# Kernel tuning notes

Hardware: AMD Instinct MI355X
Metric: run time of the kernel (lower is better)

## Reference

```python
import jax, jax.numpy as jnp
import numpy as np

NUM_INPUTS = 16
NUM_HIDDEN = 256
NUM_LAYERS = 4
B = 16384


def setup_inputs() -> dict:
    key = jax.random.key(0)
    ks = jax.random.split(key, 8)
    H, N, L = NUM_HIDDEN, NUM_INPUTS, NUM_LAYERS
    x0 = jax.random.normal(ks[0], (B, N), dtype=jnp.float32)
    # input layer: Linear(2 -> H)
    W_in = jax.random.normal(ks[1], (2, H), dtype=jnp.float32) * (1.0 / np.sqrt(2.0))
    b_in = jnp.zeros((H,), dtype=jnp.float32)
    # L-1 intermediate layers: Linear(2H -> H), stacked
    W_mid = jax.random.normal(ks[2], (L - 1, 2 * H, H), dtype=jnp.float32) * (1.0 / np.sqrt(2.0 * H))
    b_mid = jnp.zeros((L - 1, H), dtype=jnp.float32)
    # slater: Linear(H -> N) with xavier-normal weight, zero bias
    W_sl = jax.random.normal(ks[3], (H, N), dtype=jnp.float32) * np.sqrt(2.0 / (H + N))
    b_sl = jnp.zeros((N,), dtype=jnp.float32)
    width = jnp.full((1,), 0.1, dtype=jnp.float32)
    return {"x0": x0, "W_in": W_in, "b_in": b_in, "W_mid": W_mid,
            "b_mid": b_mid, "W_sl": W_sl, "b_sl": b_sl, "width": width}


def _forward(x0, W_in, b_in, W_mid, b_mid, W_sl, b_sl, width):
    N = x0.shape[1]
    # input equivariant layer: f = stack(h, mean(h)) -> [B, N, 2]
    g = jnp.broadcast_to(x0.mean(axis=1, keepdims=True), x0.shape)
    f = jnp.stack((x0, g), axis=2)                       # [B, N, 2]
    h = jnp.tanh(jnp.einsum('bnf,fh->bnh', f, W_in) + b_in)  # [B, N, H]
    # intermediate equivariant layers with residual
    for i in range(W_mid.shape[0]):
        gm = jnp.broadcast_to(h.mean(axis=1, keepdims=True), h.shape)
        fm = jnp.concatenate((h, gm), axis=2)            # [B, N, 2H]
        h = jnp.tanh(jnp.einsum('bnf,fh->bnh', fm, W_mid[i]) + b_mid[i]) + h
    # slog slater determinant
    slater = jnp.einsum('bnh,hm->bnm', h, W_sl) + b_sl   # [B, N, N]
    sign, logabsdet = jnp.linalg.slogdet(slater)
    log_factorial = jnp.log(jnp.arange(1, N + 1, dtype=jnp.float32)).sum()
    log_bcs = -width[0] * jnp.sum(x0 ** 2, axis=1)       # [B]
    return sign, logabsdet - 0.5 * log_factorial + log_bcs


def reference(x0, W_in, b_in, W_mid, b_mid, W_sl, b_sl, width):
    return _forward(x0, W_in, b_in, W_mid, b_mid, W_sl, b_sl, width)
```

## Files before the change

### kernel.cpp

```cpp
#include <hip/hip_runtime.h>

#define BTOT 16384
#define NI   16
#define HD   256
#define BB   4
#define NMID 3
#define ASH  264
#define SLS  20
#define HALF_LOGFACT 15.3359295387f

typedef short  bf16x8 __attribute__((ext_vector_type(8)));
typedef float  f32x4  __attribute__((ext_vector_type(4)));

__device__ __forceinline__ unsigned short f2bf(float f) {
    unsigned u = __builtin_bit_cast(unsigned, f);
    u += 0x7FFFu + ((u >> 16) & 1u);
    return (unsigned short)(u >> 16);
}
__device__ __forceinline__ unsigned cvt_pk_bf16(float lo, float hi) {
    unsigned d;
    asm("v_cvt_pk_bf16_f32 %0, %1, %2" : "=v"(d) : "v"(lo), "v"(hi));
    return d;
}
__device__ __forceinline__ float bflo(unsigned u) { return __builtin_bit_cast(float, u << 16); }
__device__ __forceinline__ float bfhi(unsigned u) { return __builtin_bit_cast(float, u & 0xFFFF0000u); }
__device__ __forceinline__ float bcast(float x, int lane) {
    return __builtin_bit_cast(float,
        __builtin_amdgcn_readlane(__builtin_bit_cast(int, x), lane));
}
__device__ __forceinline__ float tanh5(float x) {
    float z = __builtin_amdgcn_exp2f(x * 2.885390081777927f);
    return __builtin_fmaf(-2.0f, __builtin_amdgcn_rcpf(1.0f + z), 1.0f);
}
#define LGKM_BAR() do { asm volatile("s_waitcnt lgkmcnt(0)" ::: "memory"); \
    __builtin_amdgcn_s_barrier(); __builtin_amdgcn_sched_barrier(0); } while (0)
#define LGKM_WAIT() do { asm volatile("s_waitcnt lgkmcnt(0)" ::: "memory"); \
    __builtin_amdgcn_sched_barrier(0); } while (0)

__global__ void prep_w(const float* __restrict__ Wmid, const float* __restrict__ Wsl,
                       unsigned short* __restrict__ wtc) {
    const int b = blockIdx.x;
    const int t = threadIdx.x;
    unsigned short* dst = wtc + (size_t)b * 8192;
    if (b < 48) {
        const int layer = b >> 4, ch = b & 15;
        const float* src = Wmid + (size_t)layer * (2 * HD * HD);
#pragma unroll 4
        for (int v = 0; v < 32; ++v) {
            int o = t * 32 + v;
            int kk = o & 7, j = (o >> 3) & 15, kg = o >> 7;
            dst[o] = f2bf(src[(8 * kg + kk) * HD + ch * 16 + j]);
        }
    } else {
#pragma unroll 4
        for (int v = 0; v < 32; ++v) {
            int o = t * 32 + v;
            int kk = o & 7, j = (o >> 3) & 15, kg = o >> 7;
            dst[o] = (kg < 32) ? f2bf(Wsl[(8 * kg + kk) * NI + j]) : (unsigned short)0;
        }
    }
}

struct __align__(16) SMem {
    union {
        unsigned short h[BB * NI * ASH];
        float slf[BB][NI * ASH / 2];
    } u;
    unsigned short stash[2 * NI * ASH];
    unsigned short gmgv[BB * HD];
};
static_assert(sizeof(SMem) == 52736, "R6-proven 3-blocks/CU size");

__global__ __launch_bounds__(256, 3)
void eqslater_mfma(const float* __restrict__ x0g,
                   const float* __restrict__ Win,
                   const float* __restrict__ bin,
                   const float* __restrict__ bmid,
                   const float* __restrict__ bsl,
                   const float* __restrict__ width,
                   const unsigned short* __restrict__ wtc,
                   float* __restrict__ out) {
    __shared__ SMem sm;
    const int tid = threadIdx.x;
    const int bbase = blockIdx.x * BB;
    const int w = tid >> 6;
    const int l = tid & 63;
    const int c = l & 15;
    const int g = l >> 4;
    const int j4 = 4 * g;
    const int B0 = 64 * w;

    const unsigned short* wlane = wtc + (size_t)g * 128 + (size_t)c * 8;

    float x0v = x0g[bbase * NI + l];
    {
        float ssum = x0v;
#pragma unroll
        for (int off = 8; off > 0; off >>= 1) ssum += __shfl_xor(ssum, off);
        const float gme = ssum * 0.0625f;
        const int jc = B0 + l;
        const float w0 = Win[jc], w1 = Win[HD + jc], bj = bin[jc];
#pragma unroll
        for (int el = 0; el < 4; ++el) {
            float ge = bcast(gme, el * 16);
            float gl = __builtin_fmaf(ge, w1, bj);
#pragma unroll 4
            for (int r = 0; r < NI; ++r) {
                float xv = bcast(x0v, el * 16 + r);
                float f = tanh5(__builtin_fmaf(xv, w0, gl));
                sm.u.h[(el * NI + r) * ASH + jc] =
                    (unsigned short)cvt_pk_bf16(f, f);
            }
        }
    }
    LGKM_BAR();

    bf16x8 afE[2][8], wf[8], sbuf[8];

#pragma unroll 1
    for (int layer = 0; layer < NMID; ++layer) {
#pragma unroll
        for (int el = 0; el < 2; ++el)
#pragma unroll
            for (int s = 0; s < 8; ++s)
                afE[el][s] = *(const bf16x8*)&sm.u.h[(el * NI + c) * ASH + 32 * s + 8 * g];
        {
            const int r32 = tid >> 3;
            const int seg = tid & 7;
            const unsigned short* srcp = &sm.u.h[(32 + r32) * ASH + seg * 32];
            unsigned short* dstp = &sm.stash[r32 * ASH + seg * 32];
#pragma unroll
            for (int p = 0; p < 4; ++p)
                *(uint4*)(dstp + p * 8) = *(const uint4*)(srcp + p * 8);
        }
        {
            const int el2 = l >> 4;
            const int c0 = B0 + (l & 15) * 4;
            float s0 = 0, s1 = 0, s2 = 0, s3 = 0;
#pragma unroll
            for (int r = 0; r < NI; ++r) {
                uint2 d = *(const uint2*)&sm.u.h[(el2 * NI + r) * ASH + c0];
                s0 += bflo(d.x); s1 += bfhi(d.x);
                s2 += bflo(d.y); s3 += bfhi(d.y);
            }
            uint2 go;
            go.x = cvt_pk_bf16(s0 * 0.0625f, s1 * 0.0625f);
            go.y = cvt_pk_bf16(s2 * 0.0625f, s3 * 0.0625f);
            *(uint2*)&sm.gmgv[el2 * HD + c0] = go;
        }
        LGKM_BAR();

#pragma unroll
        for (int s = 0; s < 8; ++s)
            sbuf[s] = *(const bf16x8*)&sm.gmgv[(c & 3) * HD + 32 * s + 8 * g];
        LGKM_BAR();

        const float* bml = bmid + layer * HD;

#pragma unroll
        for (int cc = 0; cc < 4; ++cc) {
            const int ch = 4 * w + cc;
            const unsigned short* cb2 = wlane + (size_t)(layer * 16 + ch) * 8192 + 4096;
#pragma unroll
            for (int s = 0; s < 8; ++s)
                wf[s] = *(const bf16x8*)(cb2 + s * 512);
            f32x4 accG = {0.f, 0.f, 0.f, 0.f};
#pragma unroll
            for (int s = 0; s < 8; ++s)
                accG = __builtin_amdgcn_mfma_f32_16x16x32_bf16(wf[s], sbuf[s], accG, 0, 0, 0);
            const float4 bv = *(const float4*)&bml[ch * 16 + j4];
            if (c < 4) {
                uint2 go;
                go.x = cvt_pk_bf16(accG[0] + bv.x, accG[1] + bv.y);
                go.y = cvt_pk_bf16(accG[2] + bv.z, accG[3] + bv.w);
                *(uint2*)&sm.gmgv[c * HD + ch * 16 + j4] = go;
            }
        }
        LGKM_WAIT();

#pragma unroll
        for (int cc = 0; cc < 4; ++cc) {
            const int ch = 4 * w + cc;
            const unsigned short* cb = wlane + (size_t)(layer * 16 + ch) * 8192;
#pragma unroll
            for (int s = 0; s < 8; ++s)
                wf[s] = *(const bf16x8*)(cb + s * 512);

#pragma unroll
            for (int el = 0; el < 2; ++el) {
                f32x4 acc = {0.f, 0.f, 0.f, 0.f};
#pragma unroll
                for (int s = 0; s < 8; ++s)
                    acc = __builtin_amdgcn_mfma_f32_16x16x32_bf16(wf[s], afE[el][s], acc, 0, 0, 0);
                const uint2 gd = *(const uint2*)&sm.gmgv[el * HD + ch * 16 + j4];
                unsigned short* hrow = &sm.u.h[(el * NI + c) * ASH + ch * 16 + j4];
                uint2 hd2 = *(const uint2*)hrow;
                float f0 = tanh5(acc[0] + bflo(gd.x)) + bflo(hd2.x);
                float f1 = tanh5(acc[1] + bfhi(gd.x)) + bfhi(hd2.x);
                float f2 = tanh5(acc[2] + bflo(gd.y)) + bflo(hd2.y);
                float f3 = tanh5(acc[3] + bfhi(gd.y)) + bfhi(hd2.y);
                uint2 wo; wo.x = cvt_pk_bf16(f0, f1); wo.y = cvt_pk_bf16(f2, f3);
                *(uint2*)hrow = wo;
            }
#pragma unroll
            for (int el = 2; el < 4; ++el) {
#pragma unroll
                for (int s = 0; s < 8; ++s)
                    sbuf[s] = *(const bf16x8*)&sm.stash[((el - 2) * NI + c) * ASH + 32 * s + 8 * g];
                f32x4 acc = {0.f, 0.f, 0.f, 0.f};
#pragma unroll
                for (int s = 0; s < 8; ++s)
                    acc = __builtin_amdgcn_mfma_f32_16x16x32_bf16(wf[s], sbuf[s], acc, 0, 0, 0);
                const uint2 gd = *(const uint2*)&sm.gmgv[el * HD + ch * 16 + j4];
                unsigned short* hrow = &sm.u.h[(el * NI + c) * ASH + ch * 16 + j4];
                uint2 hd2 = *(const uint2*)hrow;
                float f0 = tanh5(acc[0] + bflo(gd.x)) + bflo(hd2.x);
                float f1 = tanh5(acc[1] + bfhi(gd.x)) + bfhi(hd2.x);
                float f2 = tanh5(acc[2] + bflo(gd.y)) + bflo(hd2.y);
                float f3 = tanh5(acc[3] + bfhi(gd.y)) + bfhi(hd2.y);
                uint2 wo; wo.x = cvt_pk_bf16(f0, f1); wo.y = cvt_pk_bf16(f2, f3);
                *(uint2*)hrow = wo;
            }
        }
        LGKM_BAR();
    }

    {
        const int e = w;
#pragma unroll
        for (int s = 0; s < 8; ++s)
            sbuf[s] = *(const bf16x8*)&sm.u.h[(e * NI + c) * ASH + 32 * s + 8 * g];
        const unsigned short* cb = wlane + (size_t)48 * 8192;
        f32x4 a0 = {0.f,0.f,0.f,0.f}, a1 = {0.f,0.f,0.f,0.f};
#pragma unroll
        for (int s = 0; s < 4; ++s) {
            bf16x8 b0 = *(const bf16x8*)(cb + (2 * s) * 512);
            bf16x8 b1 = *(const bf16x8*)(cb + (2 * s + 1) * 512);
            a0 = __builtin_amdgcn_mfma_f32_16x16x32_bf16(b0, sbuf[2 * s],     a0, 0, 0, 0);
            a1 = __builtin_amdgcn_mfma_f32_16x16x32_bf16(b1, sbuf[2 * s + 1], a1, 0, 0, 0);
        }
        f32x4 sv = a0 + a1;
        const float4 bsv = *(const float4*)&bsl[j4];
        float* slp = &sm.u.slf[e][0];
        float4 o;
        o.x = sv[0] + bsv.x; o.y = sv[1] + bsv.y;
        o.z = sv[2] + bsv.z; o.w = sv[3] + bsv.w;
        *(float4*)&slp[c * SLS + j4] = o;
    }
    LGKM_WAIT();

    {
        const int e = w;
        const float* slp = &sm.u.slf[e][0];
        const int i = c;
        float M[16];
#pragma unroll
        for (int jj = 0; jj < 4; ++jj) {
            float4 vv = *(const float4*)&slp[i * SLS + 4 * jj];
            M[4 * jj] = vv.x; M[4 * jj + 1] = vv.y; M[4 * jj + 2] = vv.z; M[4 * jj + 3] = vv.w;
        }

        int elim = 0;
        unsigned chosen = 0;
        int invcnt = 0;
        float dsign = 1.f, logabs = 0.f;
#pragma unroll
        for (int k = 0; k < 16; ++k) {
            float myv = elim ? -1.f : __builtin_fabsf(M[k]);
            float maxv = myv;
#pragma unroll
            for (int off = 8; off > 0; off >>= 1)
                maxv = fmaxf(maxv, __shfl_xor(maxv, off));
            unsigned long long bal = __ballot(myv == maxv);
            const int p = (__ffsll((long long)bal) - 1) & 15;

            invcnt += __popc(chosen >> (p + 1));
            chosen |= 1u << p;
            if (i == p) elim = 1;

            float piv = bcast(M[k], p);
            float ap = fmaxf(__builtin_fabsf(piv), 1e-35f);
            logabs += __logf(ap);
            if (piv < 0.f) dsign = -dsign;
            float spiv = __builtin_copysignf(ap, piv);
            float mi = __fdividef(M[k], spiv);
#pragma unroll
            for (int j = k + 1; j < 16; ++j) {
                float pr = bcast(M[j], p);
                if (!elim) M[j] = __builtin_fmaf(-mi, pr, M[j]);
            }
        }
        if (invcnt & 1) dsign = -dsign;

        float xv = (l < NI) ? x0g[(bbase + w) * NI + l] : 0.f;
        float sq = xv * xv;
#pragma unroll
        for (int off = 8; off > 0; off >>= 1) sq += __shfl_xor(sq, off);

        if (l == 0) {
            out[bbase + w] = dsign;
            out[BTOT + bbase + w] = logabs - HALF_LOGFACT - width[0] * sq;
        }
    }
}

extern "C" void kernel_launch(void* const* d_in, const int* in_sizes, int n_in,
                              void* d_out, int out_size, void* d_ws, size_t ws_size,
                              hipStream_t stream) {
    const float* x0   = (const float*)d_in[0];
    const float* Win  = (const float*)d_in[1];
    const float* bin  = (const float*)d_in[2];
    const float* Wmid = (const float*)d_in[3];
    const float* bmid = (const float*)d_in[4];
    const float* Wsl  = (const float*)d_in[5];
    const float* bsl  = (const float*)d_in[6];
    const float* wid  = (const float*)d_in[7];
    float* out = (float*)d_out;

    unsigned short* wtc = (unsigned short*)d_ws;

    hipLaunchKernelGGL(prep_w, dim3(49), dim3(256), 0, stream, Wmid, Wsl, wtc);
    hipLaunchKernelGGL(eqslater_mfma, dim3(BTOT / BB), dim3(256), 0, stream,
                       x0, Win, bin, bmid, bsl, wid, wtc, out);
}
```

Before: 251.9 us.

## Restructure mid-layer MFMA loops to cut register pressure and interleave accumulators

```diff
diff --git a/kernel.cpp b/kernel.cpp
--- a/kernel.cpp
+++ b/kernel.cpp
@@ -115,15 +115,10 @@
     }
     LGKM_BAR();
 
-    bf16x8 afE[2][8], wf[8], sbuf[8];
+    bf16x8 afE[2][8], sbufG[8];
 
 #pragma unroll 1
     for (int layer = 0; layer < NMID; ++layer) {
-#pragma unroll
-        for (int el = 0; el < 2; ++el)
-#pragma unroll
-            for (int s = 0; s < 8; ++s)
-                afE[el][s] = *(const bf16x8*)&sm.u.h[(el * NI + c) * ASH + 32 * s + 8 * g];
         {
             const int r32 = tid >> 3;
             const int seg = tid & 7;
@@ -152,22 +147,26 @@
 
 #pragma unroll
         for (int s = 0; s < 8; ++s)
-            sbuf[s] = *(const bf16x8*)&sm.gmgv[(c & 3) * HD + 32 * s + 8 * g];
+            sbufG[s] = *(const bf16x8*)&sm.gmgv[(c & 3) * HD + 32 * s + 8 * g];
         LGKM_BAR();
 
         const float* bml = bmid + layer * HD;
 
-#pragma unroll
+#pragma unroll 1
         for (int cc = 0; cc < 4; ++cc) {
             const int ch = 4 * w + cc;
             const unsigned short* cb2 = wlane + (size_t)(layer * 16 + ch) * 8192 + 4096;
-#pragma unroll
-            for (int s = 0; s < 8; ++s)
-                wf[s] = *(const bf16x8*)(cb2 + s * 512);
             f32x4 accG = {0.f, 0.f, 0.f, 0.f};
 #pragma unroll
-            for (int s = 0; s < 8; ++s)
-                accG = __builtin_amdgcn_mfma_f32_16x16x32_bf16(wf[s], sbuf[s], accG, 0, 0, 0);
+            for (int half = 0; half < 2; ++half) {
+                bf16x8 wfh[4];
+#pragma unroll
+                for (int s = 0; s < 4; ++s)
+                    wfh[s] = *(const bf16x8*)(cb2 + (4 * half + s) * 512);
+#pragma unroll
+                for (int s = 0; s < 4; ++s)
+                    accG = __builtin_amdgcn_mfma_f32_16x16x32_bf16(wfh[s], sbufG[4 * half + s], accG, 0, 0, 0);
+            }
             const float4 bv = *(const float4*)&bml[ch * 16 + j4];
             if (c < 4) {
                 uint2 go;
@@ -176,22 +175,47 @@
                 *(uint2*)&sm.gmgv[c * HD + ch * 16 + j4] = go;
             }
         }
-        LGKM_WAIT();
-
-#pragma unroll
+
+#pragma unroll
+        for (int el = 0; el < 2; ++el)
+#pragma unroll
+            for (int s = 0; s < 8; ++s)
+                afE[el][s] = *(const bf16x8*)&sm.u.h[(el * NI + c) * ASH + 32 * s + 8 * g];
+        LGKM_BAR();
+
+#pragma unroll 1
         for (int cc = 0; cc < 4; ++cc) {
             const int ch = 4 * w + cc;
             const unsigned short* cb = wlane + (size_t)(layer * 16 + ch) * 8192;
-#pragma unroll
-            for (int s = 0; s < 8; ++s)
-                wf[s] = *(const bf16x8*)(cb + s * 512);
-
-#pragma unroll
-            for (int el = 0; el < 2; ++el) {
-                f32x4 acc = {0.f, 0.f, 0.f, 0.f};
-#pragma unroll
-                for (int s = 0; s < 8; ++s)
-                    acc = __builtin_amdgcn_mfma_f32_16x16x32_bf16(wf[s], afE[el][s], acc, 0, 0, 0);
+            f32x4 acc0 = {0.f,0.f,0.f,0.f}, acc1 = {0.f,0.f,0.f,0.f};
+            f32x4 acc2 = {0.f,0.f,0.f,0.f}, acc3 = {0.f,0.f,0.f,0.f};
+#pragma unroll
+            for (int half = 0; half < 2; ++half) {
+                bf16x8 wfh[4], sb[4];
+#pragma unroll
+                for (int s = 0; s < 4; ++s)
+                    wfh[s] = *(const bf16x8*)(cb + (4 * half + s) * 512);
+#pragma unroll
+                for (int s = 0; s < 4; ++s) {
+                    acc0 = __builtin_amdgcn_mfma_f32_16x16x32_bf16(wfh[s], afE[0][4 * half + s], acc0, 0, 0, 0);
+                    acc1 = __builtin_amdgcn_mfma_f32_16x16x32_bf16(wfh[s], afE[1][4 * half + s], acc1, 0, 0, 0);
+                }
+#pragma unroll
+                for (int s = 0; s < 4; ++s)
+                    sb[s] = *(const bf16x8*)&sm.stash[c * ASH + 32 * (4 * half + s) + 8 * g];
+#pragma unroll
+                for (int s = 0; s < 4; ++s)
+                    acc2 = __builtin_amdgcn_mfma_f32_16x16x32_bf16(wfh[s], sb[s], acc2, 0, 0, 0);
+#pragma unroll
+                for (int s = 0; s < 4; ++s)
+                    sb[s] = *(const bf16x8*)&sm.stash[(NI + c) * ASH + 32 * (4 * half + s) + 8 * g];
+#pragma unroll
+                for (int s = 0; s < 4; ++s)
+                    acc3 = __builtin_amdgcn_mfma_f32_16x16x32_bf16(wfh[s], sb[s], acc3, 0, 0, 0);
+            }
+#pragma unroll
+            for (int el = 0; el < 4; ++el) {
+                f32x4 acc = (el == 0) ? acc0 : (el == 1) ? acc1 : (el == 2) ? acc2 : acc3;
                 const uint2 gd = *(const uint2*)&sm.gmgv[el * HD + ch * 16 + j4];
                 unsigned short* hrow = &sm.u.h[(el * NI + c) * ASH + ch * 16 + j4];
                 uint2 hd2 = *(const uint2*)hrow;
@@ -202,42 +226,24 @@
                 uint2 wo; wo.x = cvt_pk_bf16(f0, f1); wo.y = cvt_pk_bf16(f2, f3);
                 *(uint2*)hrow = wo;
             }
-#pragma unroll
-            for (int el = 2; el < 4; ++el) {
-#pragma unroll
-                for (int s = 0; s < 8; ++s)
-                    sbuf[s] = *(const bf16x8*)&sm.stash[((el - 2) * NI + c) * ASH + 32 * s + 8 * g];
-                f32x4 acc = {0.f, 0.f, 0.f, 0.f};
-#pragma unroll
-                for (int s = 0; s < 8; ++s)
-                    acc = __builtin_amdgcn_mfma_f32_16x16x32_bf16(wf[s], sbuf[s], acc, 0, 0, 0);
-                const uint2 gd = *(const uint2*)&sm.gmgv[el * HD + ch * 16 + j4];
-                unsigned short* hrow = &sm.u.h[(el * NI + c) * ASH + ch * 16 + j4];
-                uint2 hd2 = *(const uint2*)hrow;
-                float f0 = tanh5(acc[0] + bflo(gd.x)) + bflo(hd2.x);
-                float f1 = tanh5(acc[1] + bfhi(gd.x)) + bfhi(hd2.x);
-                float f2 = tanh5(acc[2] + bflo(gd.y)) + bflo(hd2.y);
-                float f3 = tanh5(acc[3] + bfhi(gd.y)) + bfhi(hd2.y);
-                uint2 wo; wo.x = cvt_pk_bf16(f0, f1); wo.y = cvt_pk_bf16(f2, f3);
-                *(uint2*)hrow = wo;
-            }
         }
         LGKM_BAR();
     }
 
     {
         const int e = w;
+        bf16x8 sb8[8];
 #pragma unroll
         for (int s = 0; s < 8; ++s)
-            sbuf[s] = *(const bf16x8*)&sm.u.h[(e * NI + c) * ASH + 32 * s + 8 * g];
+            sb8[s] = *(const bf16x8*)&sm.u.h[(e * NI + c) * ASH + 32 * s + 8 * g];
         const unsigned short* cb = wlane + (size_t)48 * 8192;
         f32x4 a0 = {0.f,0.f,0.f,0.f}, a1 = {0.f,0.f,0.f,0.f};
 #pragma unroll
         for (int s = 0; s < 4; ++s) {
             bf16x8 b0 = *(const bf16x8*)(cb + (2 * s) * 512);
             bf16x8 b1 = *(const bf16x8*)(cb + (2 * s + 1) * 512);
-            a0 = __builtin_amdgcn_mfma_f32_16x16x32_bf16(b0, sbuf[2 * s],     a0, 0, 0, 0);
-            a1 = __builtin_amdgcn_mfma_f32_16x16x32_bf16(b1, sbuf[2 * s + 1], a1, 0, 0, 0);
+            a0 = __builtin_amdgcn_mfma_f32_16x16x32_bf16(b0, sb8[2 * s],     a0, 0, 0, 0);
+            a1 = __builtin_amdgcn_mfma_f32_16x16x32_bf16(b1, sb8[2 * s + 1], a1, 0, 0, 0);
         }
         f32x4 sv = a0 + a1;
         const float4 bsv = *(const float4*)&bsl[j4];
```

After: 249.0 us. About the same (-1.1%).
